# Optimization experiments

Measured on AMD Instinct MI355X. Metric: run time of the kernel, lower is better.

The kernel has to match this reference:

```python
import jax, jax.numpy as jnp
import numpy as np

N_SUBJECTS = 16
N_LABELS = 8
DENS_TEMP = 0.1  # args.ProtoSim_dens_temp


def setup_inputs() -> dict:
    key = jax.random.key(0)
    k1, k2, k3 = jax.random.split(key, 3)
    B, C, D = 16384, 2, 1024
    X_data = jax.random.normal(k1, (B, C, D), dtype=jnp.float32)
    subject = jax.random.randint(k2, (B,), 0, N_SUBJECTS, dtype=jnp.int64) if jax.config.jax_enable_x64 else jax.random.randint(k2, (B,), 0, N_SUBJECTS).astype(jnp.int32)
    labels = jax.random.randint(k3, (B,), 0, N_LABELS).astype(subject.dtype)
    return {"X_data": X_data, "subject": subject, "labels": labels}


def reference(X_data, subject, labels):
    B, C, D = X_data.shape
    K = N_SUBJECTS * N_LABELS  # all (subject,label) groups assumed present
    # contrast_feature = cat(unbind(X_data, 1), 0) -> [B*C, D]
    feat = X_data.swapaxes(0, 1).reshape(B * C, D)
    sub2 = jnp.tile(subject, C)          # cat((subject, subject))
    lab2 = jnp.tile(labels, C)
    # torch.unique sorts -> group g = subject * N_LABELS + label matches loop order
    gid = sub2 * N_LABELS + lab2
    counts = jax.ops.segment_sum(jnp.ones((B * C,), feat.dtype), gid, num_segments=K)  # (K,)
    centroid = jax.ops.segment_sum(feat, gid, num_segments=K) / counts[:, None]       # (K, D)
    # per-row euclidean distance to own group centroid (torch.cdist to 1 point)
    dist = jnp.linalg.norm(feat - centroid[gid], axis=1)                               # (B*C,)
    mean_sqrt = jax.ops.segment_sum(jnp.sqrt(dist), gid, num_segments=K) / counts
    density = mean_sqrt / jnp.log(counts + 10.0)
    density = jnp.where(counts <= 1.0, density.max(), density)
    density = jnp.clip(density, jnp.quantile(density, 0.1), jnp.quantile(density, 0.9))
    density = DENS_TEMP * density / density.mean()                                     # (K,)
    # masks: positives = same label, different subject
    g_sub = jnp.arange(K) // N_LABELS
    g_lab = jnp.arange(K) % N_LABELS
    subj_mask = (sub2[:, None] != g_sub[None, :]).astype(feat.dtype)  # (B*C, K)
    lab_mask = (lab2[:, None] == g_lab[None, :]).astype(feat.dtype)
    mask = subj_mask * lab_mask
    # every row has N_SUBJECTS-1 positives (all groups present), so no row filtering
    sim = (feat @ centroid.T) / density[None, :]                                        # (B*C, K)
    sim = sim - sim.max(axis=1, keepdims=True)
    pos = sim * mask
    logp = jax.nn.log_softmax(pos, axis=1)
    row_loss = -(mask * logp).sum(axis=1) / mask.sum(axis=1)  # soft-target CE / #pos
    return row_loss.reshape(C, B).mean()
```

## Files before the change

### kernel.cpp

```cpp
#include <hip/hip_runtime.h>
#include <hip/hip_bf16.h>
#include <math.h>

#define NSUB 16
#define NLAB 8
#define KG 128
#define BN 16384
#define DD 1024

typedef float v4f __attribute__((ext_vector_type(4)));
typedef short short8v __attribute__((ext_vector_type(8)));

static __device__ __forceinline__ short f2bf(float f) {
    unsigned u = __builtin_bit_cast(unsigned, f);
    unsigned r = (u + 0x7fffu + ((u >> 16) & 1u)) >> 16;
    return (short)r;
}

static __device__ __forceinline__ float bf2f(unsigned short u) {
    unsigned v = ((unsigned)u) << 16;
    return __builtin_bit_cast(float, v);
}

static __device__ __forceinline__ short8v pack_bf8(float4 lo, float4 hi) {
    union { short8v s; __hip_bfloat162 h[4]; } u;
    u.h[0] = __float22bfloat162_rn(float2{lo.x, lo.y});
    u.h[1] = __float22bfloat162_rn(float2{lo.z, lo.w});
    u.h[2] = __float22bfloat162_rn(float2{hi.x, hi.y});
    u.h[3] = __float22bfloat162_rn(float2{hi.z, hi.w});
    return u.s;
}

static __device__ __forceinline__ float dot4(float4 v) {
    return v.x * v.x + v.y * v.y + v.z * v.z + v.w * v.w;
}

__global__ __launch_bounds__(1024) void k0_gid(const int* __restrict__ subject,
                                               const int* __restrict__ labels,
                                               int* __restrict__ gid, int* __restrict__ hist) {
    __shared__ int h[KG];
    int t = threadIdx.x;
    if (t < KG) h[t] = 0;
    __syncthreads();
    int b = blockIdx.x * 1024 + t;
    int g = subject[b] * NLAB + labels[b];
    gid[b] = g;
    atomicAdd(&h[g], 1);
    __syncthreads();
    if (t < KG) hist[blockIdx.x * KG + t] = h[t];
}

__global__ __launch_bounds__(1024) void k0c_scatter(const int* __restrict__ gid,
                                                    const int* __restrict__ hist,
                                                    int* __restrict__ cnt,
                                                    int* __restrict__ rowlist) {
    __shared__ int tots[KG], base0[KG], lcur[KG];
    int t = threadIdx.x, bi = blockIdx.x;
    if (t < KG) {
        int tot = 0, pre = 0;
#pragma unroll
        for (int j = 0; j < 16; ++j) {
            int v = hist[j * KG + t];
            tot += v;
            if (j < bi) pre += v;
        }
        tots[t] = tot;
        base0[t] = pre;
        lcur[t] = 0;
        if (bi == 0) cnt[t] = tot;
    }
    __syncthreads();
    if (t < KG) {
        int o = 0;
        for (int j = 0; j < t; ++j) o += tots[j];
        base0[t] += o;
    }
    __syncthreads();
    int b = bi * 1024 + t;
    int g = gid[b];
    rowlist[base0[g] + atomicAdd(&lcur[g], 1)] = b;
}

__global__ __launch_bounds__(256) void k1_centroid(const float* __restrict__ X,
                                                   const int* __restrict__ rowlist,
                                                   const int* __restrict__ cnt,
                                                   unsigned short* __restrict__ Cbf,
                                                   float* __restrict__ cnormPart) {
    int g = blockIdx.x >> 1;
    int half = blockIdx.x & 1;
    int t = threadIdx.x, lane = t & 63, w = t >> 6;
    int d = half * 512 + t * 2;
    __shared__ int rows[512];
    __shared__ int sh_no[2];
    __shared__ float wsum[4];
    if (w == 0) {
        int v = 0;
        if (lane < g) v += cnt[lane];
        if (lane + 64 < g) v += cnt[lane + 64];
#pragma unroll
        for (int x = 32; x; x >>= 1) v += __shfl_xor(v, x, 64);
        if (lane == 0) { sh_no[0] = v; sh_no[1] = cnt[g]; }
    }
    __syncthreads();
    int o = sh_no[0], n = min(sh_no[1], 512);
    for (int i = t; i < n; i += 256) rows[i] = rowlist[o + i];
    __syncthreads();
    float ax = 0.f, ay = 0.f;
    int i = 0;
    for (; i + 16 <= n; i += 16) {
        float2 v[32];
#pragma unroll
        for (int u = 0; u < 16; ++u) {
            size_t base = (size_t)rows[i + u] * 2048 + d;
            v[2 * u] = *(const float2*)(X + base);
            v[2 * u + 1] = *(const float2*)(X + base + 1024);
        }
#pragma unroll
        for (int u = 0; u < 32; ++u) { ax += v[u].x; ay += v[u].y; }
    }
    for (; i < n; ++i) {
        size_t base = (size_t)rows[i] * 2048 + d;
        float2 v0 = *(const float2*)(X + base);
        float2 v1 = *(const float2*)(X + base + 1024);
        ax += v0.x + v1.x; ay += v0.y + v1.y;
    }
    float inv = 1.f / (2.f * (float)n);
    float cx = ax * inv, cy = ay * inv;
    ushort2 cb = make_ushort2((unsigned short)f2bf(cx), (unsigned short)f2bf(cy));
    *(ushort2*)(Cbf + (size_t)g * DD + d) = cb;
    float s = cx * cx + cy * cy;
#pragma unroll
    for (int x = 32; x; x >>= 1) s += __shfl_xor(s, x, 64);
    if (lane == 0) wsum[w] = s;
    __syncthreads();
    if (t == 0) cnormPart[half * KG + g] = wsum[0] + wsum[1] + wsum[2] + wsum[3];
}

__global__ __launch_bounds__(256) void k5a_dot(const float* __restrict__ X,
                                               const unsigned short* __restrict__ Cbf,
                                               const int* __restrict__ gid,
                                               const float* __restrict__ cnormPart,
                                               unsigned short* __restrict__ Dotb,
                                               float* __restrict__ sqsPart) {
    __shared__ float h[KG];
    __shared__ float cnormS[KG];
    int t = threadIdx.x, lane = t & 63;
    if (t < KG) {
        h[t] = 0.f;
        cnormS[t] = cnormPart[t] + cnormPart[KG + t];
    }
    __syncthreads();
    int gw = blockIdx.x * 4 + (t >> 6);
    int row0 = gw * 32;
    int m = lane & 15, q = lane >> 4;
    int r0 = row0 + m, r1 = row0 + 16 + m;
    const float* a0p = X + (size_t)(r0 & (BN - 1)) * 2048 + (size_t)(r0 >> 14) * 1024 + q * 8;
    const float* a1p = X + (size_t)(r1 & (BN - 1)) * 2048 + (size_t)(r1 >> 14) * 1024 + q * 8;
    const unsigned short* bp = Cbf + (size_t)m * DD + q * 8;

    v4f acc[2][8];
#pragma unroll
    for (int i = 0; i < 2; ++i)
#pragma unroll
        for (int j = 0; j < 8; ++j) acc[i][j] = (v4f){0.f, 0.f, 0.f, 0.f};

    float s0 = 0.f, s1 = 0.f;
    short8v caA0, caA1, caB0, caB1, cbA[8], cbB[8];
    {
        float4 t0l = *(const float4*)(a0p), t0h = *(const float4*)(a0p + 4);
        float4 t1l = *(const float4*)(a1p), t1h = *(const float4*)(a1p + 4);
        s0 += dot4(t0l) + dot4(t0h); s1 += dot4(t1l) + dot4(t1h);
        caA0 = pack_bf8(t0l, t0h); caA1 = pack_bf8(t1l, t1h);
        float4 u0l = *(const float4*)(a0p + 32), u0h = *(const float4*)(a0p + 36);
        float4 u1l = *(const float4*)(a1p + 32), u1h = *(const float4*)(a1p + 36);
        s0 += dot4(u0l) + dot4(u0h); s1 += dot4(u1l) + dot4(u1h);
        caB0 = pack_bf8(u0l, u0h); caB1 = pack_bf8(u1l, u1h);
#pragma unroll
        for (int gt = 0; gt < 8; ++gt) {
            cbA[gt] = *(const short8v*)(bp + gt * 16 * DD);
            cbB[gt] = *(const short8v*)(bp + gt * 16 * DD + 32);
        }
    }
    float4 pA0l = *(const float4*)(a0p + 64), pA0h = *(const float4*)(a0p + 68);
    float4 pA1l = *(const float4*)(a1p + 64), pA1h = *(const float4*)(a1p + 68);
    float4 pB0l = *(const float4*)(a0p + 96), pB0h = *(const float4*)(a0p + 100);
    float4 pB1l = *(const float4*)(a1p + 96), pB1h = *(const float4*)(a1p + 100);

    for (int kc = 0; kc < 32; kc += 2) {
        {
            int kb = (kc + 2 <= 31 ? kc + 2 : 31) * 32;
            short8v nb[8];
#pragma unroll
            for (int gt = 0; gt < 8; ++gt) nb[gt] = *(const short8v*)(bp + gt * 16 * DD + kb);
#pragma unroll
            for (int gt = 0; gt < 8; ++gt) {
                acc[0][gt] = __builtin_amdgcn_mfma_f32_16x16x32_bf16(caA0, cbA[gt], acc[0][gt], 0, 0, 0);
                acc[1][gt] = __builtin_amdgcn_mfma_f32_16x16x32_bf16(caA1, cbA[gt], acc[1][gt], 0, 0, 0);
            }
            if (kc < 30) {
                s0 += dot4(pA0l) + dot4(pA0h); s1 += dot4(pA1l) + dot4(pA1h);
                caA0 = pack_bf8(pA0l, pA0h); caA1 = pack_bf8(pA1l, pA1h);
                int kf = (kc + 4 <= 31 ? kc + 4 : 0) * 32;
                pA0l = *(const float4*)(a0p + kf); pA0h = *(const float4*)(a0p + kf + 4);
                pA1l = *(const float4*)(a1p + kf); pA1h = *(const float4*)(a1p + kf + 4);
            }
#pragma unroll
            for (int gt = 0; gt < 8; ++gt) cbA[gt] = nb[gt];
        }
        {
            int kb = (kc + 3 <= 31 ? kc + 3 : 31) * 32;
            short8v nb[8];
#pragma unroll
            for (int gt = 0; gt < 8; ++gt) nb[gt] = *(const short8v*)(bp + gt * 16 * DD + kb);
#pragma unroll
            for (int gt = 0; gt < 8; ++gt) {
                acc[0][gt] = __builtin_amdgcn_mfma_f32_16x16x32_bf16(caB0, cbB[gt], acc[0][gt], 0, 0, 0);
                acc[1][gt] = __builtin_amdgcn_mfma_f32_16x16x32_bf16(caB1, cbB[gt], acc[1][gt], 0, 0, 0);
            }
            if (kc < 30) {
                s0 += dot4(pB0l) + dot4(pB0h); s1 += dot4(pB1l) + dot4(pB1h);
                caB0 = pack_bf8(pB0l, pB0h); caB1 = pack_bf8(pB1l, pB1h);
                int kf = (kc + 5 <= 31 ? kc + 5 : 0) * 32;
                pB0l = *(const float4*)(a0p + kf); pB0h = *(const float4*)(a0p + kf + 4);
                pB1l = *(const float4*)(a1p + kf); pB1h = *(const float4*)(a1p + kf + 4);
            }
#pragma unroll
            for (int gt = 0; gt < 8; ++gt) cbB[gt] = nb[gt];
        }
    }

    s0 += __shfl_xor(s0, 16, 64); s0 += __shfl_xor(s0, 32, 64);
    s1 += __shfl_xor(s1, 16, 64); s1 += __shfl_xor(s1, 32, 64);

#pragma unroll
    for (int tile = 0; tile < 2; ++tile)
#pragma unroll
        for (int reg = 0; reg < 4; ++reg) {
            int row = row0 + tile * 16 + q * 4 + reg;
            int b = row & (BN - 1);
            int g = gid[b];
            float own = 0.f;
#pragma unroll
            for (int gt = 0; gt < 8; ++gt) {
                float v = acc[tile][gt][reg];
                Dotb[(size_t)row * KG + gt * 16 + m] = (unsigned short)f2bf(v);
                if ((g >> 4) == gt) own = v;
            }
            float rn = __shfl(tile ? s1 : s0, q * 4 + reg, 64);
            if ((g & 15) == m) {
                float d2 = fmaxf(rn - 2.f * own + cnormS[g], 0.f);
                atomicAdd(&h[g], sqrtf(sqrtf(d2)));
            }
        }
    __syncthreads();
    if (t < KG) sqsPart[(size_t)blockIdx.x * KG + t] = h[t];
}

__global__ __launch_bounds__(256) void k5b_loss(const unsigned short* __restrict__ Dotb,
                                                const int* __restrict__ gid,
                                                const float* __restrict__ sqsPart,
                                                const int* __restrict__ cnt,
                                                float* __restrict__ out) {
    __shared__ float tmp[KG], d1s[KG], qv[4];
    __shared__ float recipDen[KG];
    __shared__ float wsum[4];
    int t = threadIdx.x;
    float cntf = 0.f, d0 = 0.f, v = 0.f;
    if (t < KG) {
        float ss = 0.f;
        for (int j = 0; j < 256; j += 4)
            ss += sqsPart[(size_t)j * KG + t] + sqsPart[(size_t)(j + 1) * KG + t] +
                  sqsPart[(size_t)(j + 2) * KG + t] + sqsPart[(size_t)(j + 3) * KG + t];
        cntf = 2.f * (float)cnt[t];
        d0 = (ss / cntf) / logf(cntf + 10.f);
        tmp[t] = d0;
    }
    __syncthreads();
    if (t < KG) {
        float dmax = -INFINITY;
        for (int j = 0; j < KG; ++j) dmax = fmaxf(dmax, tmp[j]);
        v = (cntf <= 1.f) ? dmax : d0;
        d1s[t] = v;
    }
    __syncthreads();
    if (t < KG) {
        int less = 0, eq = 0;
        for (int j = 0; j < KG; ++j) {
            float u = d1s[j];
            less += (u < v) ? 1 : 0;
            eq += (u == v) ? 1 : 0;
        }
        const int ppos[4] = {12, 13, 114, 115};
        for (int qq = 0; qq < 4; ++qq)
            if (less <= ppos[qq] && ppos[qq] < less + eq) qv[qq] = v;
    }
    __syncthreads();
    if (t < KG) {
        float q10 = 0.3f * qv[0] + 0.7f * qv[1];
        float q90 = 0.7f * qv[2] + 0.3f * qv[3];
        tmp[t] = fminf(fmaxf(v, q10), q90);
    }
    __syncthreads();
    if (t < KG) {
        float sum = 0.f;
        for (int j = 0; j < KG; ++j) sum += tmp[j];
        float mean = sum / (float)KG;
        recipDen[t] = mean / (0.1f * tmp[t]);
    }
    __syncthreads();
    int row = blockIdx.x * 256 + t;
    int b = row & (BN - 1);
    int g = gid[b];
    int s = g >> 3, l = g & 7;
    const short8v* dp = (const short8v*)(Dotb + (size_t)row * KG);
    float mx = -INFINITY;
    float psave[16];
#pragma unroll
    for (int c = 0; c < 16; ++c) {
        short8v dv = dp[c];
        const float* rv = &recipDen[c * 8];
        float x[8];
#pragma unroll
        for (int j = 0; j < 8; ++j) {
            x[j] = bf2f((unsigned short)dv[j]) * rv[j];
            mx = fmaxf(mx, x[j]);
        }
        float sel = x[0];
#pragma unroll
        for (int j = 1; j < 8; ++j) sel = (j == l) ? x[j] : sel;
        psave[c] = sel;
    }
    float S = 0.f, P = 0.f;
#pragma unroll
    for (int j = 0; j < 16; ++j) {
        float pv = psave[j] - mx;
        float e = expf(pv);
        bool use = (j != s);
        S += use ? e : 0.f;
        P += use ? pv : 0.f;
    }
    float ll = logf(113.f + S) - P * (1.f / 15.f);
#pragma unroll
    for (int x = 32; x; x >>= 1) ll += __shfl_xor(ll, x, 64);
    int lane = t & 63, w = t >> 6;
    if (lane == 0) wsum[w] = ll;
    __syncthreads();
    if (t == 0) atomicAdd(out, (wsum[0] + wsum[1] + wsum[2] + wsum[3]) * (1.f / 32768.f));
}

extern "C" void kernel_launch(void* const* d_in, const int* in_sizes, int n_in,
                              void* d_out, int out_size, void* d_ws, size_t ws_size,
                              hipStream_t stream) {
    const float* X = (const float*)d_in[0];
    const int* subject = (const int*)d_in[1];
    const int* labels = (const int*)d_in[2];
    float* out = (float*)d_out;
    char* w = (char*)d_ws;
    int* gid = (int*)(w + 0);
    int* hist = (int*)(w + 65536);
    int* cnt = (int*)(w + 73728);
    float* cnormPart = (float*)(w + 74240);
    int* rowlist = (int*)(w + 131072);
    unsigned short* Cbf = (unsigned short*)(w + 262144);
    float* sqsPart = (float*)(w + 524288);
    unsigned short* Dotb = (unsigned short*)(w + 2097152);

    hipMemsetAsync(out, 0, sizeof(float), stream);

    k0_gid<<<16, 1024, 0, stream>>>(subject, labels, gid, hist);
    k0c_scatter<<<16, 1024, 0, stream>>>(gid, hist, cnt, rowlist);
    k1_centroid<<<KG * 2, 256, 0, stream>>>(X, rowlist, cnt, Cbf, cnormPart);
    k5a_dot<<<256, 256, 0, stream>>>(X, Cbf, gid, cnormPart, Dotb, sqsPart);
    k5b_loss<<<128, 256, 0, stream>>>(Dotb, gid, sqsPart, cnt, out);
}
```

Baseline: 267.5 us.

## Emit pre-tiled bf16 copy of X in centroid pass for MFMA dot kernel

The centroid kernel now writes a bf16 copy of the input features in an MFMA-fragment tiled layout, and the centroids in the same tiled format. The dot kernel streams these contiguous tiles with a 4-deep register prefetch instead of re-reading strided fp32 rows and converting them. Dotb is stored in a blocked layout read by a retuned loss kernel. This trades an extra 64 MB scattered write for halved, coalesced reads in the GEMM. Row norms are now computed from bf16-rounded values.

```diff
diff --git a/kernel.cpp b/kernel.cpp
--- a/kernel.cpp
+++ b/kernel.cpp
@@ -10,6 +10,7 @@
 
 typedef float v4f __attribute__((ext_vector_type(4)));
 typedef short short8v __attribute__((ext_vector_type(8)));
+typedef unsigned short ushort4v __attribute__((ext_vector_type(4)));
 
 static __device__ __forceinline__ short f2bf(float f) {
     unsigned u = __builtin_bit_cast(unsigned, f);
@@ -22,17 +23,10 @@
     return __builtin_bit_cast(float, v);
 }
 
-static __device__ __forceinline__ short8v pack_bf8(float4 lo, float4 hi) {
-    union { short8v s; __hip_bfloat162 h[4]; } u;
-    u.h[0] = __float22bfloat162_rn(float2{lo.x, lo.y});
-    u.h[1] = __float22bfloat162_rn(float2{lo.z, lo.w});
-    u.h[2] = __float22bfloat162_rn(float2{hi.x, hi.y});
-    u.h[3] = __float22bfloat162_rn(float2{hi.z, hi.w});
-    return u.s;
-}
-
-static __device__ __forceinline__ float dot4(float4 v) {
-    return v.x * v.x + v.y * v.y + v.z * v.z + v.w * v.w;
+static __device__ __forceinline__ unsigned packbf2(float x, float y) {
+    union { __hip_bfloat162 h; unsigned u; } c;
+    c.h = __float22bfloat162_rn(float2{x, y});
+    return c.u;
 }
 
 __global__ __launch_bounds__(1024) void k0_gid(const int* __restrict__ subject,
@@ -84,12 +78,15 @@
 __global__ __launch_bounds__(256) void k1_centroid(const float* __restrict__ X,
                                                    const int* __restrict__ rowlist,
                                                    const int* __restrict__ cnt,
-                                                   unsigned short* __restrict__ Cbf,
-                                                   float* __restrict__ cnormPart) {
+                                                   unsigned short* __restrict__ Btil,
+                                                   float* __restrict__ cnormPart,
+                                                   unsigned short* __restrict__ Atil) {
     int g = blockIdx.x >> 1;
     int half = blockIdx.x & 1;
     int t = threadIdx.x, lane = t & 63, w = t >> 6;
     int d = half * 512 + t * 2;
+    int kc = d >> 5, q = (d >> 3) & 3, jj = d & 7;
+    int base_t = kc * 512 + q * 128 + jj;
     __shared__ int rows[512];
     __shared__ int sh_no[2];
     __shared__ float wsum[4];
@@ -109,25 +106,37 @@
     int i = 0;
     for (; i + 16 <= n; i += 16) {
         float2 v[32];
+        int rb[16];
 #pragma unroll
         for (int u = 0; u < 16; ++u) {
-            size_t base = (size_t)rows[i + u] * 2048 + d;
+            rb[u] = rows[i + u];
+            size_t base = (size_t)rb[u] * 2048 + d;
             v[2 * u] = *(const float2*)(X + base);
             v[2 * u + 1] = *(const float2*)(X + base + 1024);
         }
 #pragma unroll
-        for (int u = 0; u < 32; ++u) { ax += v[u].x; ay += v[u].y; }
+        for (int u = 0; u < 16; ++u) {
+            ax += v[2 * u].x + v[2 * u + 1].x;
+            ay += v[2 * u].y + v[2 * u + 1].y;
+            size_t rm = (size_t)(rb[u] >> 4) * 16384 + (size_t)(rb[u] & 15) * 8;
+            *(unsigned*)(Atil + rm + base_t) = packbf2(v[2 * u].x, v[2 * u].y);
+            *(unsigned*)(Atil + rm + 16777216 + base_t) = packbf2(v[2 * u + 1].x, v[2 * u + 1].y);
+        }
     }
     for (; i < n; ++i) {
-        size_t base = (size_t)rows[i] * 2048 + d;
+        int b = rows[i];
+        size_t base = (size_t)b * 2048 + d;
         float2 v0 = *(const float2*)(X + base);
         float2 v1 = *(const float2*)(X + base + 1024);
         ax += v0.x + v1.x; ay += v0.y + v1.y;
+        size_t rm = (size_t)(b >> 4) * 16384 + (size_t)(b & 15) * 8;
+        *(unsigned*)(Atil + rm + base_t) = packbf2(v0.x, v0.y);
+        *(unsigned*)(Atil + rm + 16777216 + base_t) = packbf2(v1.x, v1.y);
     }
     float inv = 1.f / (2.f * (float)n);
     float cx = ax * inv, cy = ay * inv;
-    ushort2 cb = make_ushort2((unsigned short)f2bf(cx), (unsigned short)f2bf(cy));
-    *(ushort2*)(Cbf + (size_t)g * DD + d) = cb;
+    int gt = g >> 4, mc = g & 15;
+    *(unsigned*)(Btil + (size_t)gt * 16384 + mc * 8 + base_t) = packbf2(cx, cy);
     float s = cx * cx + cy * cy;
 #pragma unroll
     for (int x = 32; x; x >>= 1) s += __shfl_xor(s, x, 64);
@@ -136,8 +145,8 @@
     if (t == 0) cnormPart[half * KG + g] = wsum[0] + wsum[1] + wsum[2] + wsum[3];
 }
 
-__global__ __launch_bounds__(256) void k5a_dot(const float* __restrict__ X,
-                                               const unsigned short* __restrict__ Cbf,
+__global__ __launch_bounds__(256) void k5a_dot(const unsigned short* __restrict__ Atil,
+                                               const unsigned short* __restrict__ Btil,
                                                const int* __restrict__ gid,
                                                const float* __restrict__ cnormPart,
                                                unsigned short* __restrict__ Dotb,
@@ -153,10 +162,9 @@
     int gw = blockIdx.x * 4 + (t >> 6);
     int row0 = gw * 32;
     int m = lane & 15, q = lane >> 4;
-    int r0 = row0 + m, r1 = row0 + 16 + m;
-    const float* a0p = X + (size_t)(r0 & (BN - 1)) * 2048 + (size_t)(r0 >> 14) * 1024 + q * 8;
-    const float* a1p = X + (size_t)(r1 & (BN - 1)) * 2048 + (size_t)(r1 >> 14) * 1024 + q * 8;
-    const unsigned short* bp = Cbf + (size_t)m * DD + q * 8;
+    const unsigned short* a0 = Atil + (size_t)(gw * 2) * 16384 + lane * 8;
+    const unsigned short* a1 = a0 + 16384;
+    const unsigned short* bb = Btil + lane * 8;
 
     v4f acc[2][8];
 #pragma unroll
@@ -164,86 +172,70 @@
 #pragma unroll
         for (int j = 0; j < 8; ++j) acc[i][j] = (v4f){0.f, 0.f, 0.f, 0.f};
 
+    short8v A0[4], A1[4], Bf[4][8];
+#pragma unroll
+    for (int p = 0; p < 4; ++p) {
+        A0[p] = *(const short8v*)(a0 + p * 512);
+        A1[p] = *(const short8v*)(a1 + p * 512);
+#pragma unroll
+        for (int gt = 0; gt < 8; ++gt)
+            Bf[p][gt] = *(const short8v*)(bb + (size_t)gt * 16384 + p * 512);
+    }
     float s0 = 0.f, s1 = 0.f;
-    short8v caA0, caA1, caB0, caB1, cbA[8], cbB[8];
-    {
-        float4 t0l = *(const float4*)(a0p), t0h = *(const float4*)(a0p + 4);
-        float4 t1l = *(const float4*)(a1p), t1h = *(const float4*)(a1p + 4);
-        s0 += dot4(t0l) + dot4(t0h); s1 += dot4(t1l) + dot4(t1h);
-        caA0 = pack_bf8(t0l, t0h); caA1 = pack_bf8(t1l, t1h);
-        float4 u0l = *(const float4*)(a0p + 32), u0h = *(const float4*)(a0p + 36);
-        float4 u1l = *(const float4*)(a1p + 32), u1h = *(const float4*)(a1p + 36);
-        s0 += dot4(u0l) + dot4(u0h); s1 += dot4(u1l) + dot4(u1h);
-        caB0 = pack_bf8(u0l, u0h); caB1 = pack_bf8(u1l, u1h);
+#pragma unroll
+    for (int kc = 0; kc < 32; ++kc) {
+        const int cur = kc & 3;
+        short8v nA0, nA1, nB[8];
+        if (kc + 4 < 32) {
+            nA0 = *(const short8v*)(a0 + (kc + 4) * 512);
+            nA1 = *(const short8v*)(a1 + (kc + 4) * 512);
+#pragma unroll
+            for (int gt = 0; gt < 8; ++gt)
+                nB[gt] = *(const short8v*)(bb + (size_t)gt * 16384 + (kc + 4) * 512);
+        }
 #pragma unroll
         for (int gt = 0; gt < 8; ++gt) {
-            cbA[gt] = *(const short8v*)(bp + gt * 16 * DD);
-            cbB[gt] = *(const short8v*)(bp + gt * 16 * DD + 32);
-        }
-    }
-    float4 pA0l = *(const float4*)(a0p + 64), pA0h = *(const float4*)(a0p + 68);
-    float4 pA1l = *(const float4*)(a1p + 64), pA1h = *(const float4*)(a1p + 68);
-    float4 pB0l = *(const float4*)(a0p + 96), pB0h = *(const float4*)(a0p + 100);
-    float4 pB1l = *(const float4*)(a1p + 96), pB1h = *(const float4*)(a1p + 100);
-
-    for (int kc = 0; kc < 32; kc += 2) {
+            acc[0][gt] = __builtin_amdgcn_mfma_f32_16x16x32_bf16(A0[cur], Bf[cur][gt], acc[0][gt], 0, 0, 0);
+            acc[1][gt] = __builtin_amdgcn_mfma_f32_16x16x32_bf16(A1[cur], Bf[cur][gt], acc[1][gt], 0, 0, 0);
+        }
         {
-            int kb = (kc + 2 <= 31 ? kc + 2 : 31) * 32;
-            short8v nb[8];
-#pragma unroll
-            for (int gt = 0; gt < 8; ++gt) nb[gt] = *(const short8v*)(bp + gt * 16 * DD + kb);
-#pragma unroll
-            for (int gt = 0; gt < 8; ++gt) {
-                acc[0][gt] = __builtin_amdgcn_mfma_f32_16x16x32_bf16(caA0, cbA[gt], acc[0][gt], 0, 0, 0);
-                acc[1][gt] = __builtin_amdgcn_mfma_f32_16x16x32_bf16(caA1, cbA[gt], acc[1][gt], 0, 0, 0);
+            union { short8v s; unsigned u[4]; } ua, ub;
+            ua.s = A0[cur]; ub.s = A1[cur];
+#pragma unroll
+            for (int r = 0; r < 4; ++r) {
+                float l0 = __builtin_bit_cast(float, ua.u[r] << 16);
+                float h0 = __builtin_bit_cast(float, ua.u[r] & 0xffff0000u);
+                s0 = fmaf(l0, l0, s0); s0 = fmaf(h0, h0, s0);
+                float l1 = __builtin_bit_cast(float, ub.u[r] << 16);
+                float h1 = __builtin_bit_cast(float, ub.u[r] & 0xffff0000u);
+                s1 = fmaf(l1, l1, s1); s1 = fmaf(h1, h1, s1);
             }
-            if (kc < 30) {
-                s0 += dot4(pA0l) + dot4(pA0h); s1 += dot4(pA1l) + dot4(pA1h);
-                caA0 = pack_bf8(pA0l, pA0h); caA1 = pack_bf8(pA1l, pA1h);
-                int kf = (kc + 4 <= 31 ? kc + 4 : 0) * 32;
-                pA0l = *(const float4*)(a0p + kf); pA0h = *(const float4*)(a0p + kf + 4);
-                pA1l = *(const float4*)(a1p + kf); pA1h = *(const float4*)(a1p + kf + 4);
-            }
-#pragma unroll
-            for (int gt = 0; gt < 8; ++gt) cbA[gt] = nb[gt];
-        }
-        {
-            int kb = (kc + 3 <= 31 ? kc + 3 : 31) * 32;
-            short8v nb[8];
-#pragma unroll
-            for (int gt = 0; gt < 8; ++gt) nb[gt] = *(const short8v*)(bp + gt * 16 * DD + kb);
-#pragma unroll
-            for (int gt = 0; gt < 8; ++gt) {
-                acc[0][gt] = __builtin_amdgcn_mfma_f32_16x16x32_bf16(caB0, cbB[gt], acc[0][gt], 0, 0, 0);
-                acc[1][gt] = __builtin_amdgcn_mfma_f32_16x16x32_bf16(caB1, cbB[gt], acc[1][gt], 0, 0, 0);
-            }
-            if (kc < 30) {
-                s0 += dot4(pB0l) + dot4(pB0h); s1 += dot4(pB1l) + dot4(pB1h);
-                caB0 = pack_bf8(pB0l, pB0h); caB1 = pack_bf8(pB1l, pB1h);
-                int kf = (kc + 5 <= 31 ? kc + 5 : 0) * 32;
-                pB0l = *(const float4*)(a0p + kf); pB0h = *(const float4*)(a0p + kf + 4);
-                pB1l = *(const float4*)(a1p + kf); pB1h = *(const float4*)(a1p + kf + 4);
-            }
-#pragma unroll
-            for (int gt = 0; gt < 8; ++gt) cbB[gt] = nb[gt];
+        }
+        if (kc + 4 < 32) {
+            A0[cur] = nA0; A1[cur] = nA1;
+#pragma unroll
+            for (int gt = 0; gt < 8; ++gt) Bf[cur][gt] = nB[gt];
         }
     }
 
     s0 += __shfl_xor(s0, 16, 64); s0 += __shfl_xor(s0, 32, 64);
     s1 += __shfl_xor(s1, 16, 64); s1 += __shfl_xor(s1, 32, 64);
 
+    int rowblk = row0 >> 6, rlo = row0 & 32;
 #pragma unroll
     for (int tile = 0; tile < 2; ++tile)
 #pragma unroll
         for (int reg = 0; reg < 4; ++reg) {
-            int row = row0 + tile * 16 + q * 4 + reg;
+            int rr = rlo + tile * 16 + q * 4 + reg;
+            int row = (rowblk << 6) + rr;
             int b = row & (BN - 1);
             int g = gid[b];
             float own = 0.f;
 #pragma unroll
             for (int gt = 0; gt < 8; ++gt) {
                 float v = acc[tile][gt][reg];
-                Dotb[(size_t)row * KG + gt * 16 + m] = (unsigned short)f2bf(v);
+                size_t idx = (((size_t)rowblk * 32 + gt * 4 + (m >> 2)) * 64 + rr) * 4 + (m & 3);
+                Dotb[idx] = (unsigned short)f2bf(v);
                 if ((g >> 4) == gt) own = v;
             }
             float rn = __shfl(tile ? s1 : s0, q * 4 + reg, 64);
@@ -256,30 +248,30 @@
     if (t < KG) sqsPart[(size_t)blockIdx.x * KG + t] = h[t];
 }
 
-__global__ __launch_bounds__(256) void k5b_loss(const unsigned short* __restrict__ Dotb,
+__global__ __launch_bounds__(128) void k5b_loss(const unsigned short* __restrict__ Dotb,
                                                 const int* __restrict__ gid,
                                                 const float* __restrict__ sqsPart,
                                                 const int* __restrict__ cnt,
                                                 float* __restrict__ out) {
     __shared__ float tmp[KG], d1s[KG], qv[4];
     __shared__ float recipDen[KG];
-    __shared__ float wsum[4];
+    __shared__ float wsum[2];
     int t = threadIdx.x;
-    float cntf = 0.f, d0 = 0.f, v = 0.f;
+    float cntf = 0.f, d0v = 0.f, v = 0.f;
     if (t < KG) {
         float ss = 0.f;
         for (int j = 0; j < 256; j += 4)
             ss += sqsPart[(size_t)j * KG + t] + sqsPart[(size_t)(j + 1) * KG + t] +
                   sqsPart[(size_t)(j + 2) * KG + t] + sqsPart[(size_t)(j + 3) * KG + t];
         cntf = 2.f * (float)cnt[t];
-        d0 = (ss / cntf) / logf(cntf + 10.f);
-        tmp[t] = d0;
+        d0v = (ss / cntf) / logf(cntf + 10.f);
+        tmp[t] = d0v;
     }
     __syncthreads();
     if (t < KG) {
         float dmax = -INFINITY;
         for (int j = 0; j < KG; ++j) dmax = fmaxf(dmax, tmp[j]);
-        v = (cntf <= 1.f) ? dmax : d0;
+        v = (cntf <= 1.f) ? dmax : d0v;
         d1s[t] = v;
     }
     __syncthreads();
@@ -308,23 +300,28 @@
         recipDen[t] = mean / (0.1f * tmp[t]);
     }
     __syncthreads();
-    int row = blockIdx.x * 256 + t;
+    int row = blockIdx.x * 128 + t;
     int b = row & (BN - 1);
     int g = gid[b];
     int s = g >> 3, l = g & 7;
-    const short8v* dp = (const short8v*)(Dotb + (size_t)row * KG);
+    int lane = t & 63, w = t >> 6;
+    size_t rowblk = (size_t)(row >> 6);
+    const ushort4v* dp = (const ushort4v*)Dotb;
     float mx = -INFINITY;
     float psave[16];
 #pragma unroll
     for (int c = 0; c < 16; ++c) {
-        short8v dv = dp[c];
+        size_t i0 = (rowblk * 32 + c * 2) * 64 + lane;
+        ushort4v dv0 = dp[i0];
+        ushort4v dv1 = dp[i0 + 64];
         const float* rv = &recipDen[c * 8];
         float x[8];
 #pragma unroll
-        for (int j = 0; j < 8; ++j) {
-            x[j] = bf2f((unsigned short)dv[j]) * rv[j];
-            mx = fmaxf(mx, x[j]);
-        }
+        for (int j = 0; j < 4; ++j) x[j] = bf2f((unsigned short)dv0[j]) * rv[j];
+#pragma unroll
+        for (int j = 0; j < 4; ++j) x[4 + j] = bf2f((unsigned short)dv1[j]) * rv[4 + j];
+#pragma unroll
+        for (int j = 0; j < 8; ++j) mx = fmaxf(mx, x[j]);
         float sel = x[0];
 #pragma unroll
         for (int j = 1; j < 8; ++j) sel = (j == l) ? x[j] : sel;
@@ -341,11 +338,10 @@
     }
     float ll = logf(113.f + S) - P * (1.f / 15.f);
 #pragma unroll
-    for (int x = 32; x; x >>= 1) ll += __shfl_xor(ll, x, 64);
-    int lane = t & 63, w = t >> 6;
+    for (int x2 = 32; x2; x2 >>= 1) ll += __shfl_xor(ll, x2, 64);
     if (lane == 0) wsum[w] = ll;
     __syncthreads();
-    if (t == 0) atomicAdd(out, (wsum[0] + wsum[1] + wsum[2] + wsum[3]) * (1.f / 32768.f));
+    if (t == 0) atomicAdd(out, (wsum[0] + wsum[1]) * (1.f / 32768.f));
 }
 
 extern "C" void kernel_launch(void* const* d_in, const int* in_sizes, int n_in,
@@ -361,15 +357,16 @@
     int* cnt = (int*)(w + 73728);
     float* cnormPart = (float*)(w + 74240);
     int* rowlist = (int*)(w + 131072);
-    unsigned short* Cbf = (unsigned short*)(w + 262144);
-    float* sqsPart = (float*)(w + 524288);
-    unsigned short* Dotb = (unsigned short*)(w + 2097152);
-
-    hipMemsetAsync(out, 0, sizeof(float), stream);
+    float* sqsPart = (float*)(w + 262144);
+    unsigned short* Btil = (unsigned short*)(w + 524288);
+    unsigned short* Atil = (unsigned short*)(w + 2097152);
+    unsigned short* Dotb = (unsigned short*)(w + 100663296);
+
+    (void)hipMemsetAsync(out, 0, sizeof(float), stream);
 
     k0_gid<<<16, 1024, 0, stream>>>(subject, labels, gid, hist);
     k0c_scatter<<<16, 1024, 0, stream>>>(gid, hist, cnt, rowlist);
-    k1_centroid<<<KG * 2, 256, 0, stream>>>(X, rowlist, cnt, Cbf, cnormPart);
-    k5a_dot<<<256, 256, 0, stream>>>(X, Cbf, gid, cnormPart, Dotb, sqsPart);
-    k5b_loss<<<128, 256, 0, stream>>>(Dotb, gid, sqsPart, cnt, out);
-}
+    k1_centroid<<<KG * 2, 256, 0, stream>>>(X, rowlist, cnt, Btil, cnormPart, Atil);
+    k5a_dot<<<256, 256, 0, stream>>>(Atil, Btil, gid, cnormPart, Dotb, sqsPart);
+    k5b_loss<<<256, 128, 0, stream>>>(Dotb, gid, sqsPart, cnt, out);
+}
```

Measured after the change: 296.7 us. 1.11x slower.
